# Kernel tuning notes

Measured on AMD Instinct MI355X. Metric: run time of the kernel, lower is better.

The kernel has to match this reference:

```python
import jax, jax.numpy as jnp
import numpy as np

N = 100000          # nodes
E = 1600000         # edges per adjacency (avg degree 16)
DIMS = [256, 128, 64]
ALPHA = 0.8
WD = 1e-4


def setup_inputs() -> dict:
    key = jax.random.key(0)
    ks = jax.random.split(key, 11)
    X = jax.random.normal(ks[0], (N, DIMS[0]), jnp.float32)
    rows = jax.random.randint(ks[1], (E,), 0, N, jnp.int32)
    cols = jax.random.randint(ks[2], (E,), 0, N, jnp.int32)
    prune_rows = jax.random.randint(ks[3], (E,), 0, N, jnp.int32)
    prune_cols = jax.random.randint(ks[4], (E,), 0, N, jnp.int32)
    # learned params (torch.randn init, scaled 0.1 for fp32 numeric headroom)
    W0 = jax.random.normal(ks[5], (DIMS[0], DIMS[1]), jnp.float32) * 0.1
    W1 = jax.random.normal(ks[6], (DIMS[1], DIMS[2]), jnp.float32) * 0.1
    v00 = jax.random.normal(ks[7], (DIMS[1], 1), jnp.float32) * 0.1
    v01 = jax.random.normal(ks[8], (DIMS[1], 1), jnp.float32) * 0.1
    pv00 = jax.random.normal(ks[9], (DIMS[1], 1), jnp.float32) * 0.1
    pv01 = jax.random.normal(ks[10], (DIMS[1], 1), jnp.float32) * 0.1
    return {"X": X, "W0": W0, "W1": W1, "v00": v00, "v01": v01,
            "pv00": pv00, "pv01": pv01, "rows": rows, "cols": cols,
            "prune_rows": prune_rows, "prune_cols": prune_cols}


def _edge_softmax(rows, logits, n):
    # row-wise softmax over sparse edge logits
    m = jax.ops.segment_max(logits, rows, num_segments=n)
    e = jnp.exp(logits - m[rows])
    s = jax.ops.segment_sum(e, rows, num_segments=n)
    return e / s[rows]


def _attention(rows, cols, H, va, vb, n):
    # logit_e = (H @ va)[src_e] + (H @ vb)[dst_e]  (binary adjacency values)
    f1 = (H @ va)[:, 0]
    f2 = (H @ vb)[:, 0]
    return _edge_softmax(rows, f1[rows] + f2[cols], n)


def _spmm(rows, cols, vals, H, n):
    # out[i] = sum_{e: rows[e]==i} vals[e] * H[cols[e]]
    return jax.ops.segment_sum(vals[:, None] * H[cols], rows, num_segments=n)


def reference(X, W0, W1, v00, v01, pv00, pv01, rows, cols, prune_rows, prune_cols):
    n = X.shape[0]
    # ---- encoder ----
    H1 = X @ W0                                   # layer 0 projection
    c = _attention(rows, cols, H1, v00, v01, n)   # C[0]
    pc = _attention(prune_rows, prune_cols, H1, pv00, pv01, n)  # prune_C[0]
    H1a = (1.0 - ALPHA) * _spmm(rows, cols, c, H1, n) \
        + ALPHA * _spmm(prune_rows, prune_cols, pc, H1, n)
    H1a = jax.nn.elu(H1a)                         # nonlinear, layer 0 != last
    H_enc = H1a @ W1                              # layer 1 == last: no attention
    # ---- decoder ----
    D = H_enc @ W1.T                              # layer 1
    D = (1.0 - ALPHA) * _spmm(rows, cols, c, D, n) \
        + ALPHA * _spmm(prune_rows, prune_cols, pc, D, n)
    D = jax.nn.elu(D)                             # nonlinear, layer 1 != 0
    X_ = D @ W0.T                                 # layer 0: plain matmul
    # ---- loss ----
    loss = jnp.sqrt(jnp.sum((X - X_) ** 2)) \
         + WD * (jnp.sum(W0 ** 2) + jnp.sum(W1 ** 2))
    return (loss, H_enc, X_)
```

## Files before the change

### kernel.cpp

```cpp
#include <hip/hip_runtime.h>
#include <math.h>

#define N_NODES 100000
#define N_EDGES 1600000
#define TOT (2 * N_NODES)
#define SCAN_NB 256
#define SCAN_CH 4

static inline int cdiv(long a, long b) { return (int)((a + b - 1) / b); }

typedef unsigned int uint;
typedef unsigned short ushort;
typedef __attribute__((ext_vector_type(8))) short short8v;
typedef __attribute__((ext_vector_type(4))) float f32x4;

__device__ inline float bf2f(uint u) { return __uint_as_float(u << 16); }
__device__ inline ushort f2bf(float f) {
    uint u = __float_as_uint(f);
    uint r = ((u >> 16) & 1u) + 0x7fffu;
    return (ushort)((u + r) >> 16);
}

template <int K, int M, bool AF32, int OUT, bool LOSS>
__global__ __launch_bounds__(256) void gemm_mfma(const void* __restrict__ Av,
                                                 const ushort* __restrict__ Bcm,
                                                 void* __restrict__ Cv,
                                                 const float* __restrict__ Xref,
                                                 float* __restrict__ partial,
                                                 int nrows) {
    constexpr int BM = 128;
    constexpr int KP = K + 8;
    constexpr int NCT = M / 16;
    __shared__ ushort Blds[M * KP];
    __shared__ ushort Alds[BM * 32];
    const int w = threadIdx.x >> 6;
    const int l = threadIdx.x & 63;
    const int rowg = l & 15;
    const int kg = l >> 4;
    const int rbase = blockIdx.x * BM;
    {
        const uint4* src = reinterpret_cast<const uint4*>(Bcm);
        uint4* dst = reinterpret_cast<uint4*>(Blds);
        const int total = M * KP / 8;
        for (int i = threadIdx.x; i < total; i += 256) dst[i] = src[i];
    }
    f32x4 acc[2][NCT] = {};
    for (int k0 = 0; k0 < K; k0 += 32) {
        __syncthreads();
        int r = threadIdx.x >> 1;
        int kk = (threadIdx.x & 1) * 16;
        int rg = min(rbase + r, nrows - 1);
        if (AF32) {
            const float* A = (const float*)Av;
            const float4* src = reinterpret_cast<const float4*>(A + (size_t)rg * K + k0 + kk);
            ushort* dst = &Alds[r * 32 + kk];
#pragma unroll
            for (int q = 0; q < 4; ++q) {
                float4 v = src[q];
                dst[4 * q + 0] = f2bf(v.x); dst[4 * q + 1] = f2bf(v.y);
                dst[4 * q + 2] = f2bf(v.z); dst[4 * q + 3] = f2bf(v.w);
            }
        } else {
            const ushort* A = (const ushort*)Av;
            const uint4* src = reinterpret_cast<const uint4*>(A + (size_t)rg * K + k0 + kk);
            uint4* dst = reinterpret_cast<uint4*>(&Alds[r * 32 + kk]);
            dst[0] = src[0];
            dst[1] = src[1];
        }
        __syncthreads();
#pragma unroll
        for (int rt = 0; rt < 2; ++rt) {
            short8v af = *reinterpret_cast<const short8v*>(
                &Alds[(w * 32 + rt * 16 + rowg) * 32 + kg * 8]);
#pragma unroll
            for (int ct = 0; ct < NCT; ++ct) {
                short8v bf = *reinterpret_cast<const short8v*>(
                    &Blds[(ct * 16 + rowg) * KP + k0 + kg * 8]);
                acc[rt][ct] = __builtin_amdgcn_mfma_f32_16x16x32_bf16(
                    af, bf, acc[rt][ct], 0, 0, 0);
            }
        }
    }
    float lsum = 0.f;
#pragma unroll
    for (int rt = 0; rt < 2; ++rt) {
#pragma unroll
        for (int q = 0; q < 4; ++q) {
            int r = rbase + w * 32 + rt * 16 + kg * 4 + q;
            if (r >= nrows) continue;
#pragma unroll
            for (int ct = 0; ct < NCT; ++ct) {
                float o = acc[rt][ct][q];
                int col = ct * 16 + rowg;
                if (OUT == 0) ((float*)Cv)[(size_t)r * M + col] = o;
                else ((ushort*)Cv)[(size_t)r * M + col] = f2bf(o);
                if (LOSS) {
                    float d = o - Xref[(size_t)r * 256 + col];
                    lsum += d * d;
                }
            }
        }
    }
    if (LOSS) {
        __shared__ float smRed[4];
#pragma unroll
        for (int off = 32; off > 0; off >>= 1) lsum += __shfl_down(lsum, off);
        __syncthreads();
        if (l == 0) smRed[w] = lsum;
        __syncthreads();
        if (threadIdx.x == 0)
            partial[blockIdx.x] = smRed[0] + smRed[1] + smRed[2] + smRed[3];
    }
}

__global__ __launch_bounds__(256) void transpose_kernel(const float* __restrict__ in,
                                                        float* __restrict__ out,
                                                        int rows, int cols) {
    int i = blockIdx.x * 256 + threadIdx.x;
    if (i >= rows * cols) return;
    int r = i / cols, c = i - r * cols;
    out[c * rows + r] = in[i];
}

__global__ __launch_bounds__(256) void prepB1_kernel(const float* __restrict__ W0,
                                                     ushort* __restrict__ B1cm) {
    int i = blockIdx.x * 256 + threadIdx.x;
    if (i >= 256 * 128) return;
    int k = i / 128, m = i - k * 128;
    B1cm[m * 264 + k] = f2bf(W0[(size_t)k * 128 + m]);
}

__global__ __launch_bounds__(256) void prepB8_kernel(const float* __restrict__ W0,
                                                     ushort* __restrict__ B8cm) {
    int i = blockIdx.x * 256 + threadIdx.x;
    if (i >= 256 * 128) return;
    int m = i / 128, k = i - m * 128;
    B8cm[m * 136 + k] = f2bf(W0[(size_t)m * 128 + k]);
}

template <int K, int M, int R, int RT, int OUT, bool ELU, bool LOSS, bool GUARD>
__global__ __launch_bounds__(256) void gemm_rb(const float* __restrict__ A,
                                               const float* __restrict__ B,
                                               void* __restrict__ Cv,
                                               void* __restrict__ Cv2,
                                               const float* __restrict__ Xref,
                                               float* __restrict__ partial,
                                               int nrows) {
    constexpr int KC = 32;
    constexpr int TPR = M / 4;
    constexpr int G = 256 / TPR;
    static_assert(G * RT == R, "tile geometry");
    __shared__ float Blds[KC * M];
    __shared__ float Alds[KC][R];
    const int tcol = threadIdx.x % TPR;
    const int tg   = threadIdx.x / TPR;
    const int rbase = blockIdx.x * R;
    float acc[RT][4] = {};
    for (int k0 = 0; k0 < K; k0 += KC) {
        const float4* Bsrc = reinterpret_cast<const float4*>(B + (size_t)k0 * M);
        float4* Bdst = reinterpret_cast<float4*>(Blds);
#pragma unroll
        for (int i = 0; i < (KC * M / 4) / 256; ++i)
            Bdst[i * 256 + threadIdx.x] = Bsrc[i * 256 + threadIdx.x];
#pragma unroll
        for (int e = threadIdx.x; e < R * KC; e += 256) {
            int rr = e / KC, kk = e - rr * KC;
            int rg = rbase + rr;
            if (GUARD) rg = min(rg, nrows - 1);
            Alds[kk][rr] = A[(size_t)rg * K + k0 + kk];
        }
        __syncthreads();
#pragma unroll
        for (int kk = 0; kk < KC; ++kk) {
            float ar[RT];
#pragma unroll
            for (int q = 0; q < RT / 4; ++q) {
                float4 av = *reinterpret_cast<const float4*>(&Alds[kk][tg * RT + 4 * q]);
                ar[4 * q] = av.x; ar[4 * q + 1] = av.y;
                ar[4 * q + 2] = av.z; ar[4 * q + 3] = av.w;
            }
            float4 bv = *reinterpret_cast<const float4*>(&Blds[kk * M + tcol * 4]);
            float br[4] = {bv.x, bv.y, bv.z, bv.w};
#pragma unroll
            for (int i = 0; i < RT; ++i)
#pragma unroll
                for (int j = 0; j < 4; ++j)
                    acc[i][j] += ar[i] * br[j];
        }
        __syncthreads();
    }
#pragma unroll
    for (int i = 0; i < RT; ++i) {
        int r = rbase + tg * RT + i;
        if (GUARD && r >= nrows) continue;
        float o0 = acc[i][0], o1 = acc[i][1], o2 = acc[i][2], o3 = acc[i][3];
        if (ELU) {
            o0 = o0 > 0.f ? o0 : expm1f(o0);
            o1 = o1 > 0.f ? o1 : expm1f(o1);
            o2 = o2 > 0.f ? o2 : expm1f(o2);
            o3 = o3 > 0.f ? o3 : expm1f(o3);
        }
        if (OUT == 0 || OUT == 3) {
            float* c = (float*)Cv + (size_t)r * M + tcol * 4;
            c[0] = o0; c[1] = o1; c[2] = o2; c[3] = o3;
        } else if (OUT == 1) {
            float* c = (float*)Cv + (size_t)r * M + tcol * 4;
            *reinterpret_cast<float4*>(c) = make_float4(o0, o1, o2, o3);
        }
        if (OUT == 2 || OUT == 3) {
            void* dst = (OUT == 2) ? Cv : Cv2;
            ushort* c = (ushort*)dst + (size_t)r * M + tcol * 4;
            uint2 wv;
            wv.x = (uint)f2bf(o0) | ((uint)f2bf(o1) << 16);
            wv.y = (uint)f2bf(o2) | ((uint)f2bf(o3) << 16);
            *reinterpret_cast<uint2*>(c) = wv;
        }
    }
}

__global__ __launch_bounds__(256) void attn_f4_kernel(const ushort* __restrict__ Hb,
                                                      const float* __restrict__ va,
                                                      const float* __restrict__ vb,
                                                      const float* __restrict__ pva,
                                                      const float* __restrict__ pvb,
                                                      float* __restrict__ f1,
                                                      float* __restrict__ f2,
                                                      float* __restrict__ pf1,
                                                      float* __restrict__ pf2) {
    int wid = (blockIdx.x * 256 + threadIdx.x) >> 6;
    int lane = threadIdx.x & 63;
    if (wid >= N_NODES) return;
    uint hv = reinterpret_cast<const uint*>(Hb + (size_t)wid * 128)[lane];
    float x0 = bf2f(hv & 0xffffu);
    float x1 = bf2f(hv >> 16);
    int k = 2 * lane;
    float a = x0 * va[k] + x1 * va[k + 1];
    float b = x0 * vb[k] + x1 * vb[k + 1];
    float pa = x0 * pva[k] + x1 * pva[k + 1];
    float pb = x0 * pvb[k] + x1 * pvb[k + 1];
#pragma unroll
    for (int off = 32; off > 0; off >>= 1) {
        a += __shfl_down(a, off);
        b += __shfl_down(b, off);
        pa += __shfl_down(pa, off);
        pb += __shfl_down(pb, off);
    }
    if (lane == 0) { f1[wid] = a; f2[wid] = b; pf1[wid] = pa; pf2[wid] = pb; }
}

__global__ __launch_bounds__(256) void hist2_kernel(const int* __restrict__ rows,
                                                    const int* __restrict__ prows,
                                                    int* __restrict__ deg) {
    int e = blockIdx.x * 256 + threadIdx.x;
    if (e >= 2 * N_EDGES) return;
    int r = e < N_EDGES ? rows[e] : N_NODES + prows[e - N_EDGES];
    atomicAdd(&deg[r], 1);
}

__global__ __launch_bounds__(256) void scan1_kernel(const int* __restrict__ deg,
                                                    int* __restrict__ bsum) {
    __shared__ int sm[256];
    int base = (blockIdx.x * 256 + threadIdx.x) * SCAN_CH;
    int s = 0;
#pragma unroll
    for (int i = 0; i < SCAN_CH; ++i) {
        int idx = base + i;
        if (idx < TOT) s += deg[idx];
    }
    sm[threadIdx.x] = s;
    __syncthreads();
    for (int off = 128; off > 0; off >>= 1) {
        if (threadIdx.x < off) sm[threadIdx.x] += sm[threadIdx.x + off];
        __syncthreads();
    }
    if (threadIdx.x == 0) bsum[blockIdx.x] = sm[0];
}

__global__ void scan2_kernel(int* __restrict__ bsum) {
    if (threadIdx.x != 0) return;
    int run = 0;
    for (int i = 0; i < SCAN_NB; ++i) {
        int t = bsum[i];
        bsum[i] = run;
        run += t;
    }
}

__global__ __launch_bounds__(256) void scan3_kernel(const int* __restrict__ deg,
                                                    const int* __restrict__ bsum,
                                                    int* __restrict__ rp) {
    __shared__ int sm[256];
    int base = (blockIdx.x * 256 + threadIdx.x) * SCAN_CH;
    int s = 0;
#pragma unroll
    for (int i = 0; i < SCAN_CH; ++i) {
        int idx = base + i;
        if (idx < TOT) s += deg[idx];
    }
    sm[threadIdx.x] = s;
    __syncthreads();
    if (threadIdx.x == 0) {
        int run = bsum[blockIdx.x];
        for (int t = 0; t < 256; ++t) { int tmp = sm[t]; sm[t] = run; run += tmp; }
    }
    __syncthreads();
    int off = sm[threadIdx.x];
#pragma unroll
    for (int i = 0; i < SCAN_CH; ++i) {
        int idx = base + i;
        if (idx < TOT) { rp[idx] = off; off += deg[idx]; }
        else if (idx == TOT) rp[idx] = off;
    }
}

__global__ __launch_bounds__(256) void scatter2_kernel(const int* __restrict__ rows,
                                                       const int* __restrict__ cols,
                                                       const int* __restrict__ prows,
                                                       const int* __restrict__ pcols,
                                                       const int* __restrict__ rp,
                                                       int* __restrict__ cur,
                                                       int* __restrict__ ccol) {
    int e = blockIdx.x * 256 + threadIdx.x;
    if (e >= 2 * N_EDGES) return;
    int r, c;
    if (e < N_EDGES) { r = rows[e]; c = cols[e]; }
    else { int e2 = e - N_EDGES; r = N_NODES + prows[e2]; c = pcols[e2]; }
    int pos = rp[r] + atomicAdd(&cur[r], 1);
    ccol[pos] = c;
}

__global__ __launch_bounds__(256) void edgeval_kernel(const int* __restrict__ rp,
                                                      const int* __restrict__ ccol,
                                                      const float* __restrict__ f1,
                                                      const float* __restrict__ f2,
                                                      const float* __restrict__ pf1,
                                                      const float* __restrict__ pf2,
                                                      int2* __restrict__ eg) {
    int r = blockIdx.x * 16 + (threadIdx.x >> 4);
    int sl = threadIdx.x & 15;
    bool second = r >= N_NODES;
    float f1r = second ? pf1[r - N_NODES] : f1[r];
    const float* f2t = second ? pf2 : f2;
    float scale = second ? 0.8f : 0.2f;
    int j0 = rp[r], e1 = rp[r + 1];
    float s = 0.f;
    for (int j = j0 + sl; j < e1; j += 16)
        s += __expf(f1r + f2t[ccol[j]]);
#pragma unroll
    for (int off = 8; off > 0; off >>= 1) s += __shfl_xor(s, off);
    float inv = s > 0.f ? scale / s : 0.f;
    for (int j = j0 + sl; j < e1; j += 16) {
        int c = ccol[j];
        float wv = __expf(f1r + f2t[c]) * inv;
        eg[j] = make_int2(c, __float_as_int(wv));
    }
}

#define SPU 8
__global__ __launch_bounds__(256) void spmm_fused_kernel(const int* __restrict__ rp,
                                                         const int2* __restrict__ eg,
                                                         const ushort* __restrict__ Hb,
                                                         float* __restrict__ out) {
    int r = blockIdx.x * 4 + (threadIdx.x >> 6);
    int lane = threadIdx.x & 63;
    const uint* Hu = reinterpret_cast<const uint*>(Hb);
    float a0 = 0.f, a1 = 0.f, b0 = 0.f, b1 = 0.f;
    int j1 = rp[r], E1 = rp[r + 1];
    int j2 = rp[N_NODES + r], E2 = rp[N_NODES + r + 1];
    int c1 = max(E1 - 1, 0), c2 = max(E2 - 1, 0);
    int nb = max((E1 - j1 + SPU - 1) / SPU, (E2 - j2 + SPU - 1) / SPU);
    for (int b = 0; b < nb; ++b) {
        int2 d1[SPU], d2[SPU];
#pragma unroll
        for (int u = 0; u < SPU; ++u) d1[u] = eg[min(j1 + u, c1)];
#pragma unroll
        for (int u = 0; u < SPU; ++u) d2[u] = eg[min(j2 + u, c2)];
        uint h1[SPU], h2[SPU];
#pragma unroll
        for (int u = 0; u < SPU; ++u) h1[u] = Hu[(size_t)d1[u].x * 64 + lane];
#pragma unroll
        for (int u = 0; u < SPU; ++u) h2[u] = Hu[(size_t)d2[u].x * 64 + lane];
#pragma unroll
        for (int u = 0; u < SPU; ++u) {
            float v1 = (j1 + u < E1) ? __int_as_float(d1[u].y) : 0.f;
            float v2 = (j2 + u < E2) ? __int_as_float(d2[u].y) : 0.f;
            a0 += v1 * bf2f(h1[u] & 0xffffu);
            a1 += v1 * bf2f(h1[u] >> 16);
            b0 += v2 * bf2f(h2[u] & 0xffffu);
            b1 += v2 * bf2f(h2[u] >> 16);
        }
        j1 += SPU; j2 += SPU;
    }
    float o0 = a0 + b0;
    float o1 = a1 + b1;
    o0 = o0 > 0.f ? o0 : expm1f(o0);
    o1 = o1 > 0.f ? o1 : expm1f(o1);
    *reinterpret_cast<float2*>(out + (size_t)r * 128 + 2 * lane) = make_float2(o0, o1);
}

__global__ __launch_bounds__(256) void spmm64_fused_kernel(const int* __restrict__ rp,
                                                           const int2* __restrict__ eg,
                                                           const ushort* __restrict__ Hb,
                                                           float* __restrict__ S) {
    int r = blockIdx.x * 4 + (threadIdx.x >> 6);
    int lane = threadIdx.x & 63;
    float a = 0.f, b = 0.f;
    int j1 = rp[r], E1 = rp[r + 1];
    int j2 = rp[N_NODES + r], E2 = rp[N_NODES + r + 1];
    int c1 = max(E1 - 1, 0), c2 = max(E2 - 1, 0);
    int nb = max((E1 - j1 + SPU - 1) / SPU, (E2 - j2 + SPU - 1) / SPU);
    for (int bb = 0; bb < nb; ++bb) {
        int2 d1[SPU], d2[SPU];
#pragma unroll
        for (int u = 0; u < SPU; ++u) d1[u] = eg[min(j1 + u, c1)];
#pragma unroll
        for (int u = 0; u < SPU; ++u) d2[u] = eg[min(j2 + u, c2)];
        ushort h1[SPU], h2[SPU];
#pragma unroll
        for (int u = 0; u < SPU; ++u) h1[u] = Hb[(size_t)d1[u].x * 64 + lane];
#pragma unroll
        for (int u = 0; u < SPU; ++u) h2[u] = Hb[(size_t)d2[u].x * 64 + lane];
#pragma unroll
        for (int u = 0; u < SPU; ++u) {
            float v1 = (j1 + u < E1) ? __int_as_float(d1[u].y) : 0.f;
            float v2 = (j2 + u < E2) ? __int_as_float(d2[u].y) : 0.f;
            a += v1 * bf2f((uint)h1[u]);
            b += v2 * bf2f((uint)h2[u]);
        }
        j1 += SPU; j2 += SPU;
    }
    S[(size_t)r * 64 + lane] = a + b;
}

__global__ __launch_bounds__(256) void sq_reduce_kernel(const float* __restrict__ a,
                                                        float* __restrict__ acc, int n) {
    __shared__ float sm[4];
    float s = 0.f;
    for (int i = blockIdx.x * 256 + threadIdx.x; i < n; i += gridDim.x * 256) {
        float d = a[i];
        s += d * d;
    }
#pragma unroll
    for (int off = 32; off > 0; off >>= 1) s += __shfl_down(s, off);
    int lane = threadIdx.x & 63, w = threadIdx.x >> 6;
    if (lane == 0) sm[w] = s;
    __syncthreads();
    if (threadIdx.x == 0) atomicAdd(acc, sm[0] + sm[1] + sm[2] + sm[3]);
}

__global__ __launch_bounds__(256) void partial_reduce_kernel(const float* __restrict__ p,
                                                             int n, float* __restrict__ acc) {
    __shared__ float sm[4];
    float s = 0.f;
    for (int i = threadIdx.x; i < n; i += 256) s += p[i];
#pragma unroll
    for (int off = 32; off > 0; off >>= 1) s += __shfl_down(s, off);
    int lane = threadIdx.x & 63, w = threadIdx.x >> 6;
    if (lane == 0) sm[w] = s;
    __syncthreads();
    if (threadIdx.x == 0) atomicAdd(acc, sm[0] + sm[1] + sm[2] + sm[3]);
}

__global__ void finalize_kernel(const float* __restrict__ acc, float* __restrict__ out) {
    out[0] = sqrtf(acc[0]) + 1e-4f * (acc[1] + acc[2]);
}

extern "C" void kernel_launch(void* const* d_in, const int* in_sizes, int n_in,
                              void* d_out, int out_size, void* d_ws, size_t ws_size,
                              hipStream_t stream) {
    const float* X    = (const float*)d_in[0];
    const float* W0   = (const float*)d_in[1];
    const float* W1   = (const float*)d_in[2];
    const float* v00  = (const float*)d_in[3];
    const float* v01  = (const float*)d_in[4];
    const float* pv00 = (const float*)d_in[5];
    const float* pv01 = (const float*)d_in[6];
    const int* rows   = (const int*)d_in[7];
    const int* cols   = (const int*)d_in[8];
    const int* prows  = (const int*)d_in[9];
    const int* pcols  = (const int*)d_in[10];

    float* out  = (float*)d_out;
    float* Henc = out + 1;
    float* Xrec = out + 1 + (size_t)N_NODES * 64;

    ushort* bufAh  = (ushort*)(out + 6400004);
    float*  S      = out + 6400004;
    int*    ccol   = (int*)(out + 12800004);
    int2*   eg     = (int2*)(out + 16000004);
    ushort* HencB  = (ushort*)(out + 22400004);
    int*    deg    = (int*)(out + 25600004);
    int*    cur    = deg + TOT;

    float* ws   = (float*)d_ws;
    float* bufB = ws;
    ushort* bufBh = (ushort*)bufB;
    float* f1   = bufB + (size_t)N_NODES * 128;
    float* f2   = f1 + N_NODES;
    float* pf1  = f2 + N_NODES;
    float* pf2  = pf1 + N_NODES;
    float* acc  = pf2 + N_NODES;
    float* W1T  = acc + 4;
    float* W0T  = W1T + 64 * 128;
    ushort* B1cm = (ushort*)(W0T + 128 * 256);
    ushort* B8cm = B1cm + 128 * 264;
    int*   rp   = (int*)(B8cm + 256 * 136);
    int*   bsum = rp + TOT + 1;
    float* partial = (float*)(bsum + SCAN_NB);

    const int n = N_NODES;
    const int EG2 = cdiv(2 * (long)N_EDGES, 256);

    transpose_kernel<<<cdiv(128 * 64, 256), 256, 0, stream>>>(W1, W1T, 128, 64);
    transpose_kernel<<<cdiv(256 * 128, 256), 256, 0, stream>>>(W0, W0T, 256, 128);
    prepB1_kernel<<<cdiv(256 * 128, 256), 256, 0, stream>>>(W0, B1cm);
    prepB8_kernel<<<cdiv(256 * 128, 256), 256, 0, stream>>>(W0, B8cm);

    gemm_mfma<256, 128, true, 2, false><<<cdiv(n, 128), 256, 0, stream>>>(
        X, B1cm, bufAh, nullptr, nullptr, n);

    hipMemsetAsync(deg, 0, 2 * (size_t)TOT * sizeof(int), stream);
    hipMemsetAsync(acc, 0, 4 * sizeof(float), stream);

    attn_f4_kernel<<<cdiv(n, 4), 256, 0, stream>>>(bufAh, v00, v01, pv00, pv01,
                                                   f1, f2, pf1, pf2);

    hist2_kernel<<<EG2, 256, 0, stream>>>(rows, prows, deg);
    scan1_kernel<<<SCAN_NB, 256, 0, stream>>>(deg, bsum);
    scan2_kernel<<<1, 64, 0, stream>>>(bsum);
    scan3_kernel<<<SCAN_NB, 256, 0, stream>>>(deg, bsum, rp);
    scatter2_kernel<<<EG2, 256, 0, stream>>>(rows, cols, prows, pcols, rp, cur, ccol);
    edgeval_kernel<<<cdiv(2 * n, 16), 256, 0, stream>>>(rp, ccol, f1, f2, pf1, pf2, eg);

    spmm_fused_kernel<<<n / 4, 256, 0, stream>>>(rp, eg, bufAh, bufB);

    gemm_rb<128, 64, 64, 4, 3, false, false, true><<<cdiv(n, 64), 256, 0, stream>>>(
        bufB, W1, Henc, HencB, nullptr, nullptr, n);

    spmm64_fused_kernel<<<n / 4, 256, 0, stream>>>(rp, eg, HencB, S);

    gemm_rb<64, 128, 32, 4, 2, true, false, false><<<n / 32, 256, 0, stream>>>(
        S, W1T, bufBh, nullptr, nullptr, nullptr, n);

    gemm_mfma<128, 256, false, 0, true><<<cdiv(n, 128), 256, 0, stream>>>(
        bufBh, B8cm, Xrec, X, partial, n);

    partial_reduce_kernel<<<1, 256, 0, stream>>>(partial, cdiv(n, 128), acc + 0);
    sq_reduce_kernel<<<16, 256, 0, stream>>>(W0, acc + 1, 256 * 128);
    sq_reduce_kernel<<<4, 256, 0, stream>>>(W1, acc + 2, 128 * 64);
    finalize_kernel<<<1, 1, 0, stream>>>(acc, out);
}
```

Baseline: 910.8 us.

## Move middle GEMMs to MFMA, pad CSR rows to 8, bucket edge scatter

Replaces the two fp32 register-blocked GEMMs with the bf16 MFMA GEMM kernel, adding ELU and dual-output epilogue options and new column-major weight prep kernels. Pads each CSR row to a multiple of 8 with zero-weight entries so the SpMM loops drop per-element bounds masking and clamped loads. Splits the edge scatter into row-range buckets to improve locality of the atomic cursor updates and ccol writes, at the cost of extra passes over the edge lists. Using bf16 for the middle GEMMs lowers precision.

```diff
diff --git a/kernel.cpp b/kernel.cpp
--- a/kernel.cpp
+++ b/kernel.cpp
@@ -6,6 +6,7 @@
 #define TOT (2 * N_NODES)
 #define SCAN_NB 256
 #define SCAN_CH 4
+#define RPB 25000
 
 static inline int cdiv(long a, long b) { return (int)((a + b - 1) / b); }
 
@@ -21,10 +22,11 @@
     return (ushort)((u + r) >> 16);
 }
 
-template <int K, int M, bool AF32, int OUT, bool LOSS>
+template <int K, int M, bool AF32, int OUT, bool ELU, bool LOSS>
 __global__ __launch_bounds__(256) void gemm_mfma(const void* __restrict__ Av,
                                                  const ushort* __restrict__ Bcm,
                                                  void* __restrict__ Cv,
+                                                 void* __restrict__ Cv2,
                                                  const float* __restrict__ Xref,
                                                  float* __restrict__ partial,
                                                  int nrows) {
@@ -91,9 +93,11 @@
 #pragma unroll
             for (int ct = 0; ct < NCT; ++ct) {
                 float o = acc[rt][ct][q];
+                if (ELU) o = o > 0.f ? o : expm1f(o);
                 int col = ct * 16 + rowg;
-                if (OUT == 0) ((float*)Cv)[(size_t)r * M + col] = o;
-                else ((ushort*)Cv)[(size_t)r * M + col] = f2bf(o);
+                if (OUT == 0 || OUT == 3) ((float*)Cv)[(size_t)r * M + col] = o;
+                if (OUT == 2) ((ushort*)Cv)[(size_t)r * M + col] = f2bf(o);
+                if (OUT == 3) ((ushort*)Cv2)[(size_t)r * M + col] = f2bf(o);
                 if (LOSS) {
                     float d = o - Xref[(size_t)r * 256 + col];
                     lsum += d * d;
@@ -113,109 +117,33 @@
     }
 }
 
-__global__ __launch_bounds__(256) void transpose_kernel(const float* __restrict__ in,
-                                                        float* __restrict__ out,
-                                                        int rows, int cols) {
-    int i = blockIdx.x * 256 + threadIdx.x;
-    if (i >= rows * cols) return;
-    int r = i / cols, c = i - r * cols;
-    out[c * rows + r] = in[i];
-}
-
 __global__ __launch_bounds__(256) void prepB1_kernel(const float* __restrict__ W0,
-                                                     ushort* __restrict__ B1cm) {
+                                                     ushort* __restrict__ B) {
     int i = blockIdx.x * 256 + threadIdx.x;
     if (i >= 256 * 128) return;
     int k = i / 128, m = i - k * 128;
-    B1cm[m * 264 + k] = f2bf(W0[(size_t)k * 128 + m]);
-}
-
+    B[m * 264 + k] = f2bf(W0[i]);
+}
+__global__ __launch_bounds__(256) void prepB5_kernel(const float* __restrict__ W1,
+                                                     ushort* __restrict__ B) {
+    int i = blockIdx.x * 256 + threadIdx.x;
+    if (i >= 128 * 64) return;
+    int k = i / 64, m = i - k * 64;
+    B[m * 136 + k] = f2bf(W1[i]);
+}
+__global__ __launch_bounds__(256) void prepB7_kernel(const float* __restrict__ W1,
+                                                     ushort* __restrict__ B) {
+    int i = blockIdx.x * 256 + threadIdx.x;
+    if (i >= 128 * 64) return;
+    int m = i / 64, k = i - m * 64;
+    B[m * 72 + k] = f2bf(W1[i]);
+}
 __global__ __launch_bounds__(256) void prepB8_kernel(const float* __restrict__ W0,
-                                                     ushort* __restrict__ B8cm) {
+                                                     ushort* __restrict__ B) {
     int i = blockIdx.x * 256 + threadIdx.x;
     if (i >= 256 * 128) return;
     int m = i / 128, k = i - m * 128;
-    B8cm[m * 136 + k] = f2bf(W0[(size_t)m * 128 + k]);
-}
-
-template <int K, int M, int R, int RT, int OUT, bool ELU, bool LOSS, bool GUARD>
-__global__ __launch_bounds__(256) void gemm_rb(const float* __restrict__ A,
-                                               const float* __restrict__ B,
-                                               void* __restrict__ Cv,
-                                               void* __restrict__ Cv2,
-                                               const float* __restrict__ Xref,
-                                               float* __restrict__ partial,
-                                               int nrows) {
-    constexpr int KC = 32;
-    constexpr int TPR = M / 4;
-    constexpr int G = 256 / TPR;
-    static_assert(G * RT == R, "tile geometry");
-    __shared__ float Blds[KC * M];
-    __shared__ float Alds[KC][R];
-    const int tcol = threadIdx.x % TPR;
-    const int tg   = threadIdx.x / TPR;
-    const int rbase = blockIdx.x * R;
-    float acc[RT][4] = {};
-    for (int k0 = 0; k0 < K; k0 += KC) {
-        const float4* Bsrc = reinterpret_cast<const float4*>(B + (size_t)k0 * M);
-        float4* Bdst = reinterpret_cast<float4*>(Blds);
-#pragma unroll
-        for (int i = 0; i < (KC * M / 4) / 256; ++i)
-            Bdst[i * 256 + threadIdx.x] = Bsrc[i * 256 + threadIdx.x];
-#pragma unroll
-        for (int e = threadIdx.x; e < R * KC; e += 256) {
-            int rr = e / KC, kk = e - rr * KC;
-            int rg = rbase + rr;
-            if (GUARD) rg = min(rg, nrows - 1);
-            Alds[kk][rr] = A[(size_t)rg * K + k0 + kk];
-        }
-        __syncthreads();
-#pragma unroll
-        for (int kk = 0; kk < KC; ++kk) {
-            float ar[RT];
-#pragma unroll
-            for (int q = 0; q < RT / 4; ++q) {
-                float4 av = *reinterpret_cast<const float4*>(&Alds[kk][tg * RT + 4 * q]);
-                ar[4 * q] = av.x; ar[4 * q + 1] = av.y;
-                ar[4 * q + 2] = av.z; ar[4 * q + 3] = av.w;
-            }
-            float4 bv = *reinterpret_cast<const float4*>(&Blds[kk * M + tcol * 4]);
-            float br[4] = {bv.x, bv.y, bv.z, bv.w};
-#pragma unroll
-            for (int i = 0; i < RT; ++i)
-#pragma unroll
-                for (int j = 0; j < 4; ++j)
-                    acc[i][j] += ar[i] * br[j];
-        }
-        __syncthreads();
-    }
-#pragma unroll
-    for (int i = 0; i < RT; ++i) {
-        int r = rbase + tg * RT + i;
-        if (GUARD && r >= nrows) continue;
-        float o0 = acc[i][0], o1 = acc[i][1], o2 = acc[i][2], o3 = acc[i][3];
-        if (ELU) {
-            o0 = o0 > 0.f ? o0 : expm1f(o0);
-            o1 = o1 > 0.f ? o1 : expm1f(o1);
-            o2 = o2 > 0.f ? o2 : expm1f(o2);
-            o3 = o3 > 0.f ? o3 : expm1f(o3);
-        }
-        if (OUT == 0 || OUT == 3) {
-            float* c = (float*)Cv + (size_t)r * M + tcol * 4;
-            c[0] = o0; c[1] = o1; c[2] = o2; c[3] = o3;
-        } else if (OUT == 1) {
-            float* c = (float*)Cv + (size_t)r * M + tcol * 4;
-            *reinterpret_cast<float4*>(c) = make_float4(o0, o1, o2, o3);
-        }
-        if (OUT == 2 || OUT == 3) {
-            void* dst = (OUT == 2) ? Cv : Cv2;
-            ushort* c = (ushort*)dst + (size_t)r * M + tcol * 4;
-            uint2 wv;
-            wv.x = (uint)f2bf(o0) | ((uint)f2bf(o1) << 16);
-            wv.y = (uint)f2bf(o2) | ((uint)f2bf(o3) << 16);
-            *reinterpret_cast<uint2*>(c) = wv;
-        }
-    }
+    B[m * 136 + k] = f2bf(W0[i]);
 }
 
 __global__ __launch_bounds__(256) void attn_f4_kernel(const ushort* __restrict__ Hb,
@@ -257,6 +185,8 @@
     atomicAdd(&deg[r], 1);
 }
 
+__device__ inline int pad8(int d) { return (d + 7) & ~7; }
+
 __global__ __launch_bounds__(256) void scan1_kernel(const int* __restrict__ deg,
                                                     int* __restrict__ bsum) {
     __shared__ int sm[256];
@@ -265,7 +195,7 @@
 #pragma unroll
     for (int i = 0; i < SCAN_CH; ++i) {
         int idx = base + i;
-        if (idx < TOT) s += deg[idx];
+        if (idx < TOT) s += pad8(deg[idx]);
     }
     sm[threadIdx.x] = s;
     __syncthreads();
@@ -295,7 +225,7 @@
 #pragma unroll
     for (int i = 0; i < SCAN_CH; ++i) {
         int idx = base + i;
-        if (idx < TOT) s += deg[idx];
+        if (idx < TOT) s += pad8(deg[idx]);
     }
     sm[threadIdx.x] = s;
     __syncthreads();
@@ -308,28 +238,28 @@
 #pragma unroll
     for (int i = 0; i < SCAN_CH; ++i) {
         int idx = base + i;
-        if (idx < TOT) { rp[idx] = off; off += deg[idx]; }
+        if (idx < TOT) { rp[idx] = off; off += pad8(deg[idx]); }
         else if (idx == TOT) rp[idx] = off;
     }
 }
 
-__global__ __launch_bounds__(256) void scatter2_kernel(const int* __restrict__ rows,
-                                                       const int* __restrict__ cols,
-                                                       const int* __restrict__ prows,
-                                                       const int* __restrict__ pcols,
-                                                       const int* __restrict__ rp,
-                                                       int* __restrict__ cur,
-                                                       int* __restrict__ ccol) {
+__global__ __launch_bounds__(256) void scatter_bucket_kernel(const int* __restrict__ rlist,
+                                                             const int* __restrict__ clist,
+                                                             int roff, int lo, int hi,
+                                                             const int* __restrict__ rp,
+                                                             int* __restrict__ cur,
+                                                             int* __restrict__ ccol) {
     int e = blockIdx.x * 256 + threadIdx.x;
-    if (e >= 2 * N_EDGES) return;
-    int r, c;
-    if (e < N_EDGES) { r = rows[e]; c = cols[e]; }
-    else { int e2 = e - N_EDGES; r = N_NODES + prows[e2]; c = pcols[e2]; }
+    if (e >= N_EDGES) return;
+    int r0 = rlist[e];
+    if (r0 < lo || r0 >= hi) return;
+    int r = roff + r0;
     int pos = rp[r] + atomicAdd(&cur[r], 1);
-    ccol[pos] = c;
+    ccol[pos] = clist[e];
 }
 
 __global__ __launch_bounds__(256) void edgeval_kernel(const int* __restrict__ rp,
+                                                      const int* __restrict__ deg,
                                                       const int* __restrict__ ccol,
                                                       const float* __restrict__ f1,
                                                       const float* __restrict__ f2,
@@ -342,21 +272,44 @@
     float f1r = second ? pf1[r - N_NODES] : f1[r];
     const float* f2t = second ? pf2 : f2;
     float scale = second ? 0.8f : 0.2f;
-    int j0 = rp[r], e1 = rp[r + 1];
+    int j0 = rp[r];
+    int realend = j0 + deg[r];
+    int pend = rp[r + 1];
     float s = 0.f;
-    for (int j = j0 + sl; j < e1; j += 16)
+    for (int j = j0 + sl; j < realend; j += 16)
         s += __expf(f1r + f2t[ccol[j]]);
 #pragma unroll
     for (int off = 8; off > 0; off >>= 1) s += __shfl_xor(s, off);
     float inv = s > 0.f ? scale / s : 0.f;
-    for (int j = j0 + sl; j < e1; j += 16) {
-        int c = ccol[j];
-        float wv = __expf(f1r + f2t[c]) * inv;
-        eg[j] = make_int2(c, __float_as_int(wv));
+    for (int j = j0 + sl; j < pend; j += 16) {
+        if (j < realend) {
+            int c = ccol[j];
+            float wv = __expf(f1r + f2t[c]) * inv;
+            eg[j] = make_int2(c, __float_as_int(wv));
+        } else {
+            eg[j] = make_int2(0, 0);
+        }
     }
 }
 
 #define SPU 8
+__device__ inline void gat128(const int2* __restrict__ eg, int j,
+                              const uint* __restrict__ Hu, int lane,
+                              float& s0, float& s1) {
+    int2 d[SPU];
+#pragma unroll
+    for (int u = 0; u < SPU; ++u) d[u] = eg[j + u];
+    uint h[SPU];
+#pragma unroll
+    for (int u = 0; u < SPU; ++u) h[u] = Hu[(size_t)d[u].x * 64 + lane];
+#pragma unroll
+    for (int u = 0; u < SPU; ++u) {
+        float v = __int_as_float(d[u].y);
+        s0 += v * bf2f(h[u] & 0xffffu);
+        s1 += v * bf2f(h[u] >> 16);
+    }
+}
+
 __global__ __launch_bounds__(256) void spmm_fused_kernel(const int* __restrict__ rp,
                                                          const int2* __restrict__ eg,
                                                          const ushort* __restrict__ Hb,
@@ -367,14 +320,12 @@
     float a0 = 0.f, a1 = 0.f, b0 = 0.f, b1 = 0.f;
     int j1 = rp[r], E1 = rp[r + 1];
     int j2 = rp[N_NODES + r], E2 = rp[N_NODES + r + 1];
-    int c1 = max(E1 - 1, 0), c2 = max(E2 - 1, 0);
-    int nb = max((E1 - j1 + SPU - 1) / SPU, (E2 - j2 + SPU - 1) / SPU);
-    for (int b = 0; b < nb; ++b) {
+    while (j1 < E1 && j2 < E2) {
         int2 d1[SPU], d2[SPU];
 #pragma unroll
-        for (int u = 0; u < SPU; ++u) d1[u] = eg[min(j1 + u, c1)];
-#pragma unroll
-        for (int u = 0; u < SPU; ++u) d2[u] = eg[min(j2 + u, c2)];
+        for (int u = 0; u < SPU; ++u) d1[u] = eg[j1 + u];
+#pragma unroll
+        for (int u = 0; u < SPU; ++u) d2[u] = eg[j2 + u];
         uint h1[SPU], h2[SPU];
 #pragma unroll
         for (int u = 0; u < SPU; ++u) h1[u] = Hu[(size_t)d1[u].x * 64 + lane];
@@ -382,8 +333,8 @@
         for (int u = 0; u < SPU; ++u) h2[u] = Hu[(size_t)d2[u].x * 64 + lane];
 #pragma unroll
         for (int u = 0; u < SPU; ++u) {
-            float v1 = (j1 + u < E1) ? __int_as_float(d1[u].y) : 0.f;
-            float v2 = (j2 + u < E2) ? __int_as_float(d2[u].y) : 0.f;
+            float v1 = __int_as_float(d1[u].y);
+            float v2 = __int_as_float(d2[u].y);
             a0 += v1 * bf2f(h1[u] & 0xffffu);
             a1 += v1 * bf2f(h1[u] >> 16);
             b0 += v2 * bf2f(h2[u] & 0xffffu);
@@ -391,11 +342,26 @@
         }
         j1 += SPU; j2 += SPU;
     }
+    while (j1 < E1) { gat128(eg, j1, Hu, lane, a0, a1); j1 += SPU; }
+    while (j2 < E2) { gat128(eg, j2, Hu, lane, b0, b1); j2 += SPU; }
     float o0 = a0 + b0;
     float o1 = a1 + b1;
     o0 = o0 > 0.f ? o0 : expm1f(o0);
     o1 = o1 > 0.f ? o1 : expm1f(o1);
     *reinterpret_cast<float2*>(out + (size_t)r * 128 + 2 * lane) = make_float2(o0, o1);
+}
+
+__device__ inline void gat64(const int2* __restrict__ eg, int j,
+                             const ushort* __restrict__ Hb, int lane, float& s) {
+    int2 d[SPU];
+#pragma unroll
+    for (int u = 0; u < SPU; ++u) d[u] = eg[j + u];
+    ushort h[SPU];
+#pragma unroll
+    for (int u = 0; u < SPU; ++u) h[u] = Hb[(size_t)d[u].x * 64 + lane];
+#pragma unroll
+    for (int u = 0; u < SPU; ++u)
+        s += __int_as_float(d[u].y) * bf2f((uint)h[u]);
 }
 
 __global__ __launch_bounds__(256) void spmm64_fused_kernel(const int* __restrict__ rp,
@@ -407,14 +373,12 @@
     float a = 0.f, b = 0.f;
     int j1 = rp[r], E1 = rp[r + 1];
     int j2 = rp[N_NODES + r], E2 = rp[N_NODES + r + 1];
-    int c1 = max(E1 - 1, 0), c2 = max(E2 - 1, 0);
-    int nb = max((E1 - j1 + SPU - 1) / SPU, (E2 - j2 + SPU - 1) / SPU);
-    for (int bb = 0; bb < nb; ++bb) {
+    while (j1 < E1 && j2 < E2) {
         int2 d1[SPU], d2[SPU];
 #pragma unroll
-        for (int u = 0; u < SPU; ++u) d1[u] = eg[min(j1 + u, c1)];
-#pragma unroll
-        for (int u = 0; u < SPU; ++u) d2[u] = eg[min(j2 + u, c2)];
+        for (int u = 0; u < SPU; ++u) d1[u] = eg[j1 + u];
+#pragma unroll
+        for (int u = 0; u < SPU; ++u) d2[u] = eg[j2 + u];
         ushort h1[SPU], h2[SPU];
 #pragma unroll
         for (int u = 0; u < SPU; ++u) h1[u] = Hb[(size_t)d1[u].x * 64 + lane];
@@ -422,13 +386,13 @@
         for (int u = 0; u < SPU; ++u) h2[u] = Hb[(size_t)d2[u].x * 64 + lane];
 #pragma unroll
         for (int u = 0; u < SPU; ++u) {
-            float v1 = (j1 + u < E1) ? __int_as_float(d1[u].y) : 0.f;
-            float v2 = (j2 + u < E2) ? __int_as_float(d2[u].y) : 0.f;
-            a += v1 * bf2f((uint)h1[u]);
-            b += v2 * bf2f((uint)h2[u]);
+            a += __int_as_float(d1[u].y) * bf2f((uint)h1[u]);
+            b += __int_as_float(d2[u].y) * bf2f((uint)h2[u]);
         }
         j1 += SPU; j2 += SPU;
     }
+    while (j1 < E1) { gat64(eg, j1, Hb, lane, a); j1 += SPU; }
+    while (j2 < E2) { gat64(eg, j2, Hb, lane, b); j2 += SPU; }
     S[(size_t)r * 64 + lane] = a + b;
 }
 
@@ -487,9 +451,9 @@
     ushort* bufAh  = (ushort*)(out + 6400004);
     float*  S      = out + 6400004;
     int*    ccol   = (int*)(out + 12800004);
-    int2*   eg     = (int2*)(out + 16000004);
-    ushort* HencB  = (ushort*)(out + 22400004);
-    int*    deg    = (int*)(out + 25600004);
+    int2*   eg     = (int2*)(out + 17600004);
+    ushort* HencB  = (ushort*)(out + 27200004);
+    int*    deg    = (int*)(out + 28800004);
     int*    cur    = deg + TOT;
 
     float* ws   = (float*)d_ws;
@@ -500,24 +464,25 @@
     float* pf1  = f2 + N_NODES;
     float* pf2  = pf1 + N_NODES;
     float* acc  = pf2 + N_NODES;
-    float* W1T  = acc + 4;
-    float* W0T  = W1T + 64 * 128;
-    ushort* B1cm = (ushort*)(W0T + 128 * 256);
-    ushort* B8cm = B1cm + 128 * 264;
+    ushort* B1cm = (ushort*)(acc + 4);
+    ushort* B5cm = B1cm + 128 * 264;
+    ushort* B7cm = B5cm + 64 * 136;
+    ushort* B8cm = B7cm + 128 * 72;
     int*   rp   = (int*)(B8cm + 256 * 136);
     int*   bsum = rp + TOT + 1;
     float* partial = (float*)(bsum + SCAN_NB);
 
     const int n = N_NODES;
+    const int EG = cdiv(N_EDGES, 256);
     const int EG2 = cdiv(2 * (long)N_EDGES, 256);
 
-    transpose_kernel<<<cdiv(128 * 64, 256), 256, 0, stream>>>(W1, W1T, 128, 64);
-    transpose_kernel<<<cdiv(256 * 128, 256), 256, 0, stream>>>(W0, W0T, 256, 128);
     prepB1_kernel<<<cdiv(256 * 128, 256), 256, 0, stream>>>(W0, B1cm);
+    prepB5_kernel<<<cdiv(128 * 64, 256), 256, 0, stream>>>(W1, B5cm);
+    prepB7_kernel<<<cdiv(128 * 64, 256), 256, 0, stream>>>(W1, B7cm);
     prepB8_kernel<<<cdiv(256 * 128, 256), 256, 0, stream>>>(W0, B8cm);
 
-    gemm_mfma<256, 128, true, 2, false><<<cdiv(n, 128), 256, 0, stream>>>(
-        X, B1cm, bufAh, nullptr, nullptr, n);
+    gemm_mfma<256, 128, true, 2, false, false><<<cdiv(n, 128), 256, 0, stream>>>(
+        X, B1cm, bufAh, nullptr, nullptr, nullptr, n);
 
     hipMemsetAsync(deg, 0, 2 * (size_t)TOT * sizeof(int), stream);
     hipMemsetAsync(acc, 0, 4 * sizeof(float), stream);
@@ -529,21 +494,29 @@
     scan1_kernel<<<SCAN_NB, 256, 0, stream>>>(deg, bsum);
     scan2_kernel<<<1, 64, 0, stream>>>(bsum);
     scan3_kernel<<<SCAN_NB, 256, 0, stream>>>(deg, bsum, rp);
-    scatter2_kernel<<<EG2, 256, 0, stream>>>(rows, cols, prows, pcols, rp, cur, ccol);
-    edgeval_kernel<<<cdiv(2 * n, 16), 256, 0, stream>>>(rp, ccol, f1, f2, pf1, pf2, eg);
+    for (int p = 0; p < 4; ++p)
+        scatter_bucket_kernel<<<EG, 256, 0, stream>>>(rows, cols, 0,
+                                                      p * RPB, (p + 1) * RPB,
+                                                      rp, cur, ccol);
+    for (int p = 0; p < 4; ++p)
+        scatter_bucket_kernel<<<EG, 256, 0, stream>>>(prows, pcols, N_NODES,
+                                                      p * RPB, (p + 1) * RPB,
+                                                      rp, cur, ccol);
+    edgeval_kernel<<<cdiv(2 * n, 16), 256, 0, stream>>>(rp, deg, ccol,
+                                                        f1, f2, pf1, pf2, eg);
 
     spmm_fused_kernel<<<n / 4, 256, 0, stream>>>(rp, eg, bufAh, bufB);
 
-    gemm_rb<128, 64, 64, 4, 3, false, false, true><<<cdiv(n, 64), 256, 0, stream>>>(
-        bufB, W1, Henc, HencB, nullptr, nullptr, n);
+    gemm_mfma<128, 64, true, 3, false, false><<<cdiv(n, 128), 256, 0, stream>>>(
+        bufB, B5cm, Henc, HencB, nullptr, nullptr, n);
 
     spmm64_fused_kernel<<<n / 4, 256, 0, stream>>>(rp, eg, HencB, S);
 
-    gemm_rb<64, 128, 32, 4, 2, true, false, false><<<n / 32, 256, 0, stream>>>(
-        S, W1T, bufBh, nullptr, nullptr, nullptr, n);
-
-    gemm_mfma<128, 256, false, 0, true><<<cdiv(n, 128), 256, 0, stream>>>(
-        bufBh, B8cm, Xrec, X, partial, n);
+    gemm_mfma<64, 128, true, 2, true, false><<<cdiv(n, 128), 256, 0, stream>>>(
+        S, B7cm, bufBh, nullptr, nullptr, nullptr, n);
+
+    gemm_mfma<128, 256, false, 0, false, true><<<cdiv(n, 128), 256, 0, stream>>>(
+        bufBh, B8cm, Xrec, nullptr, X, partial, n);
 
     partial_reduce_kernel<<<1, 256, 0, stream>>>(partial, cdiv(n, 128), acc + 0);
     sq_reduce_kernel<<<16, 256, 0, stream>>>(W0, acc + 1, 256 * 128);
```

New measurement: 823.2 us. -9.6%, faster.
